# Optimization experiments

Measured on AMD Instinct MI355X. Metric: run time of the kernel, lower is better.

The kernel has to match this reference:

```python
import jax, jax.numpy as jnp
import numpy as np

N = 50000
NEG_SLOPE = 0.2

def _gat_conv(x, src, dst, W, a_src, a_dst, bias, heads, ch):
    # x: [N, F_in]; W: [F_in, heads*ch]; a_src/a_dst: [heads, ch]
    h = (x @ W).reshape(N, heads, ch)                      # [N,H,C]
    e_src = jnp.einsum('nhc,hc->nh', h, a_src)             # [N,H]
    e_dst = jnp.einsum('nhc,hc->nh', h, a_dst)             # [N,H]
    e = jax.nn.leaky_relu(e_src[src] + e_dst[dst], NEG_SLOPE)  # [E,H]
    # segment softmax over destination nodes (self-loops guarantee nonempty segments)
    m = jax.ops.segment_max(e, dst, num_segments=N)        # [N,H]
    p = jnp.exp(e - m[dst])                                # [E,H]
    s = jax.ops.segment_sum(p, dst, num_segments=N)        # [N,H]
    alpha = p / s[dst]                                     # [E,H]
    out = jax.ops.segment_sum(h[src] * alpha[:, :, None], dst, num_segments=N)  # [N,H,C]
    return out.reshape(N, heads * ch) + bias

def _forward(x, src, dst, W1, att_src1, att_dst1, b1, W2, att_src2, att_dst2, b2):
    z = _gat_conv(x, src, dst, W1, att_src1, att_dst1, b1, heads=8, ch=32)
    z = jax.nn.elu(z)
    z = _gat_conv(z, src, dst, W2, att_src2, att_dst2, b2, heads=1, ch=256)
    z = jax.nn.elu(z)
    return z

def setup_inputs() -> dict:
    key = jax.random.key(0)
    ks = jax.random.split(key, 8)
    E = 800000
    x = jax.random.normal(ks[0], (N, 128), dtype=jnp.float32)
    edge_index = jax.random.randint(ks[1], (2, E), 0, N, dtype=jnp.int64)
    g = lambda k, shape: jax.random.normal(k, shape, dtype=jnp.float32) * (1.0 / np.sqrt(shape[0]))
    return {
        'x': x,
        'edge_index': edge_index,
        'W1': g(ks[2], (128, 256)),
        'att_src1': jax.random.normal(ks[3], (8, 32), dtype=jnp.float32) * 0.1,
        'att_dst1': jax.random.normal(ks[4], (8, 32), dtype=jnp.float32) * 0.1,
        'b1': jnp.zeros((256,), dtype=jnp.float32),
        'W2': g(ks[5], (256, 256)),
        'att_src2': jax.random.normal(ks[6], (1, 256), dtype=jnp.float32) * 0.1,
        'att_dst2': jax.random.normal(ks[7], (1, 256), dtype=jnp.float32) * 0.1,
        'b2': jnp.zeros((256,), dtype=jnp.float32),
    }

def reference(x, edge_index, W1, att_src1, att_dst1, b1, W2, att_src2, att_dst2, b2):
    # PyG GATConv default add_self_loops=True: append self-loop edges
    loops = jnp.arange(N, dtype=edge_index.dtype)
    src = jnp.concatenate([edge_index[0], loops])
    dst = jnp.concatenate([edge_index[1], loops])
    return _forward(x, src, dst, W1, att_src1, att_dst1, b1, W2, att_src2, att_dst2, b2)
```

## Files before the change

### kernel.cpp

```cpp
#include <hip/hip_runtime.h>
#include <math.h>

#define N_NODES 50000
#define N_EDGES 800000
#define ET (N_EDGES + N_NODES)
#define D 256
#define NEG_SLOPE 0.2f
#define CAP 56
#define EB ((ET + 255) / 256)
#define XCONV_B ((N_NODES * 128 / 4 + 255) / 256)
#define GEMM_BY ((N_NODES + 127) / 128)

typedef __attribute__((ext_vector_type(8))) _Float16 half8;
typedef __attribute__((ext_vector_type(8))) unsigned short ushort8;
typedef __attribute__((ext_vector_type(4))) unsigned short us4;
typedef __attribute__((ext_vector_type(4))) float f32x4;

__device__ inline unsigned short f2h(float f) {
    union { _Float16 h; unsigned short u; } v; v.h = (_Float16)f; return v.u;
}
__device__ inline float h2f(unsigned short u) {
    union { unsigned short u; _Float16 h; } v; v.u = u; return (float)v.h;
}

__device__ inline int edge_src(const int* eidx, int is32, int e) {
    if (e >= N_EDGES) return e - N_EDGES;
    return is32 ? eidx[e] : eidx[2 * e];
}
__device__ inline int edge_dst(const int* eidx, int is32, int e) {
    if (e >= N_EDGES) return e - N_EDGES;
    return is32 ? eidx[N_EDGES + e] : eidx[2 * (N_EDGES + e)];
}

__global__ __launch_bounds__(256) void init_all(const int* __restrict__ eidx,
                                                int* __restrict__ flag,
                                                int* __restrict__ cnt) {
    int b = blockIdx.x, t = threadIdx.x;
    if (b == 0) {
        __shared__ int any32;
        if (t == 0) any32 = 0;
        __syncthreads();
        int found = 0;
        #pragma unroll
        for (int k = 0; k < 4; ++k) {
            int i = t * 4 + k;
            if (eidx[2 * i + 1] != 0) found = 1;
        }
        if (found) atomicOr(&any32, 1);
        __syncthreads();
        if (t == 0) *flag = any32;
    } else {
        int base = (b - 1) * 1024 + t * 4;
        #pragma unroll
        for (int k = 0; k < 4; ++k) {
            int i = base + k;
            if (i < N_NODES) cnt[i] = 0;
        }
    }
}

__global__ __launch_bounds__(256) void scatter_prep(const int* __restrict__ eidx,
                                                    const int* __restrict__ flag,
                                                    int* __restrict__ cnt,
                                                    int* __restrict__ psrcs,
                                                    const float* __restrict__ W1,
                                                    const float* __restrict__ W2,
                                                    const float* __restrict__ as2,
                                                    const float* __restrict__ ad2,
                                                    const float* __restrict__ x,
                                                    unsigned short* __restrict__ W1t,
                                                    unsigned short* __restrict__ W2t,
                                                    float* __restrict__ was2,
                                                    float* __restrict__ wad2,
                                                    unsigned short* __restrict__ xb) {
    int b = blockIdx.x, t = threadIdx.x;
    if (b < EB) {
        int e = b * 256 + t;
        if (e < ET) {
            int is32 = *flag;
            int src = edge_src(eidx, is32, e);
            int dst = edge_dst(eidx, is32, e);
            int slot = atomicAdd(&cnt[dst], 1);
            psrcs[dst * CAP + slot] = src;
        }
        return;
    }
    b -= EB;
    if (b < 128) {
        W1t[(size_t)t * 128 + b] = f2h(W1[(size_t)b * D + t]);
    } else if (b < 384) {
        int k = b - 128;
        W2t[(size_t)t * D + k] = f2h(W2[(size_t)k * D + t]);
    } else if (b == 384) {
        float s = 0.f, d = 0.f;
        for (int j = 0; j < D; ++j) {
            float w = W2[(size_t)t * D + j];
            s += w * as2[j]; d += w * ad2[j];
        }
        was2[t] = s; wad2[t] = d;
    } else {
        int i = (b - 385) * 256 + t;
        if (i < N_NODES * 128 / 4) {
            float4 v = *(const float4*)&x[(size_t)i * 4];
            us4 o; o.x = f2h(v.x); o.y = f2h(v.y); o.z = f2h(v.z); o.w = f2h(v.w);
            *(us4*)&xb[(size_t)i * 4] = o;
        }
    }
}

template <bool EPI, bool SCORES>
__device__ void gemm_body(int bx, int by,
                          const unsigned short* __restrict__ A,
                          const unsigned short* __restrict__ Bt,
                          void* __restrict__ Cout,
                          const float* __restrict__ bias,
                          const float* __restrict__ a_src,
                          const float* __restrict__ a_dst,
                          float* __restrict__ es,
                          float* __restrict__ ed,
                          int M, int K) {
    __shared__ __align__(16) unsigned short As[128][40];
    __shared__ __align__(16) unsigned short Bs[128][40];
    int t = threadIdx.x, lane = t & 63, wid = t >> 6;
    int wm = wid >> 1, wn = wid & 1;
    int row0 = by * 128, col0 = bx * 128;
    int c15 = lane & 15;
    f32x4 acc[4][4] = {};
    int ar = t >> 1, ap = t & 1;
    for (int k0 = 0; k0 < K; k0 += 32) {
        ushort8 a0 = {0,0,0,0,0,0,0,0}, a1 = {0,0,0,0,0,0,0,0};
        if (row0 + ar < M) {
            const ushort8* p = (const ushort8*)&A[(size_t)(row0 + ar) * K + k0 + ap * 16];
            a0 = p[0]; a1 = p[1];
        }
        *(ushort8*)&As[ar][ap * 16]     = a0;
        *(ushort8*)&As[ar][ap * 16 + 8] = a1;
        const ushort8* q = (const ushort8*)&Bt[(size_t)(col0 + ar) * K + k0 + ap * 16];
        *(ushort8*)&Bs[ar][ap * 16]     = q[0];
        *(ushort8*)&Bs[ar][ap * 16 + 8] = q[1];
        __syncthreads();
        half8 af[4], bg[4];
        #pragma unroll
        for (int mi = 0; mi < 4; ++mi)
            af[mi] = *(const half8*)&As[wm * 64 + mi * 16 + c15][(lane >> 4) * 8];
        #pragma unroll
        for (int ni = 0; ni < 4; ++ni)
            bg[ni] = *(const half8*)&Bs[wn * 64 + ni * 16 + c15][(lane >> 4) * 8];
        #pragma unroll
        for (int mi = 0; mi < 4; ++mi)
            #pragma unroll
            for (int ni = 0; ni < 4; ++ni)
                acc[mi][ni] = __builtin_amdgcn_mfma_f32_16x16x32_f16(af[mi], bg[ni], acc[mi][ni], 0, 0, 0);
        __syncthreads();
    }
    float bcol[4];
    if (EPI) {
        #pragma unroll
        for (int ni = 0; ni < 4; ++ni) bcol[ni] = bias[col0 + wn * 64 + ni * 16 + c15];
    }
    #pragma unroll
    for (int mi = 0; mi < 4; ++mi) {
        int rowb = row0 + wm * 64 + mi * 16 + ((lane >> 4) << 2);
        #pragma unroll
        for (int ni = 0; ni < 4; ++ni) {
            int col = col0 + wn * 64 + ni * 16 + c15;
            #pragma unroll
            for (int r = 0; r < 4; ++r) {
                if (rowb + r >= M) continue;
                if (EPI) {
                    float v = acc[mi][ni][r] + bcol[ni];
                    v = v > 0.f ? v : __expf(v) - 1.f;
                    ((float*)Cout)[(size_t)(rowb + r) * D + col] = v;
                } else {
                    ((unsigned short*)Cout)[(size_t)(rowb + r) * D + col] = f2h(acc[mi][ni][r]);
                }
            }
        }
    }
    if (SCORES) {
        float as_[4], ad_[4];
        #pragma unroll
        for (int ni = 0; ni < 4; ++ni) {
            as_[ni] = a_src[col0 + wn * 64 + ni * 16 + c15];
            ad_[ni] = a_dst[col0 + wn * 64 + ni * 16 + c15];
        }
        int hb0 = bx * 4 + wn * 2;
        #pragma unroll
        for (int mi = 0; mi < 4; ++mi) {
            int rowb = row0 + wm * 64 + mi * 16 + ((lane >> 4) << 2);
            #pragma unroll
            for (int r = 0; r < 4; ++r) {
                float p0 = acc[mi][0][r] * as_[0] + acc[mi][1][r] * as_[1];
                float p1 = acc[mi][2][r] * as_[2] + acc[mi][3][r] * as_[3];
                float q0 = acc[mi][0][r] * ad_[0] + acc[mi][1][r] * ad_[1];
                float q1 = acc[mi][2][r] * ad_[2] + acc[mi][3][r] * ad_[3];
                #pragma unroll
                for (int msk = 1; msk < 16; msk <<= 1) {
                    p0 += __shfl_xor(p0, msk, 64);
                    p1 += __shfl_xor(p1, msk, 64);
                    q0 += __shfl_xor(q0, msk, 64);
                    q1 += __shfl_xor(q1, msk, 64);
                }
                if (c15 == 0 && rowb + r < M) {
                    es[(size_t)(rowb + r) * 8 + hb0]     = p0;
                    es[(size_t)(rowb + r) * 8 + hb0 + 1] = p1;
                    ed[(size_t)(rowb + r) * 8 + hb0]     = q0;
                    ed[(size_t)(rowb + r) * 8 + hb0 + 1] = q1;
                }
            }
        }
    }
}

__global__ __launch_bounds__(256) void gemm1_scores(const unsigned short* __restrict__ xb,
                                                    const unsigned short* __restrict__ W1t,
                                                    unsigned short* __restrict__ hb,
                                                    const float* __restrict__ a_src,
                                                    const float* __restrict__ a_dst,
                                                    float* __restrict__ es,
                                                    float* __restrict__ ed) {
    gemm_body<false, true>(blockIdx.x % 2, blockIdx.x / 2, xb, W1t, hb, nullptr,
                           a_src, a_dst, es, ed, N_NODES, 128);
}

__global__ __launch_bounds__(256) void gemm2_epi(const unsigned short* __restrict__ A,
                                                 const unsigned short* __restrict__ Bt,
                                                 float* __restrict__ Cout,
                                                 const float* __restrict__ bias) {
    gemm_body<true, false>(blockIdx.x % 2, blockIdx.x / 2, A, Bt, Cout, bias,
                           nullptr, nullptr, nullptr, nullptr, N_NODES, 256);
}

__global__ __launch_bounds__(256) void softmax_alpha8(const float* __restrict__ es,
                                                      const float* __restrict__ ed,
                                                      const int* __restrict__ cnt,
                                                      const int* __restrict__ psrcs,
                                                      unsigned short* __restrict__ alpha16) {
    int n = blockIdx.x * 4 + (threadIdx.x >> 6);
    if (n >= N_NODES) return;
    int lane = threadIdx.x & 63;
    int begin = n * CAP, end = begin + cnt[n];
    int j  = lane >> 3;
    int hd = lane & 7;
    float edn = ed[(size_t)n * 8 + hd];
    float m = -1e30f, s = 0.f;
    for (int i = begin + j; i < end; i += 8) {
        float e = es[(size_t)psrcs[i] * 8 + hd] + edn;
        e = e > 0.f ? e : NEG_SLOPE * e;
        float nm = fmaxf(m, e);
        s = s * __expf(m - nm) + __expf(e - nm);
        m = nm;
    }
    #pragma unroll
    for (int mask = 8; mask < 64; mask <<= 1) {
        float om = __shfl_xor(m, mask, 64);
        float os = __shfl_xor(s, mask, 64);
        float nm = fmaxf(m, om);
        s = s * __expf(m - nm) + os * __expf(om - nm);
        m = nm;
    }
    float inv_s = 1.f / s;
    for (int i = begin + j; i < end; i += 8) {
        float e = es[(size_t)psrcs[i] * 8 + hd] + edn;
        e = e > 0.f ? e : NEG_SLOPE * e;
        alpha16[(size_t)i * 8 + hd] = f2h(__expf(e - m) * inv_s);
    }
}

__global__ __launch_bounds__(256) void gather1(const unsigned short* __restrict__ h,
                                               const unsigned short* __restrict__ alpha16,
                                               const int* __restrict__ cnt,
                                               const int* __restrict__ psrcs,
                                               const float* __restrict__ bias,
                                               unsigned short* __restrict__ outh,
                                               const float* __restrict__ was2,
                                               const float* __restrict__ wad2,
                                               float* __restrict__ es2,
                                               float* __restrict__ ed2) {
    int n = blockIdx.x * 4 + (threadIdx.x >> 6);
    if (n >= N_NODES) return;
    int lane = threadIdx.x & 63;
    int begin = n * CAP, end = begin + cnt[n];
    int hsel = lane >> 3;
    float ax = 0.f, ay = 0.f, az = 0.f, aw = 0.f;
    int i = begin;
    for (; i + 7 < end; i += 8) {
        int ss[8]; float w[8]; us4 v[8];
        #pragma unroll
        for (int u = 0; u < 8; ++u) ss[u] = psrcs[i + u];
        #pragma unroll
        for (int u = 0; u < 8; ++u) w[u] = h2f(alpha16[(size_t)(i + u) * 8 + hsel]);
        #pragma unroll
        for (int u = 0; u < 8; ++u) v[u] = *(const us4*)&h[(size_t)ss[u] * D + lane * 4];
        #pragma unroll
        for (int u = 0; u < 8; ++u) {
            ax += h2f(v[u].x) * w[u];
            ay += h2f(v[u].y) * w[u];
            az += h2f(v[u].z) * w[u];
            aw += h2f(v[u].w) * w[u];
        }
    }
    for (; i < end; ++i) {
        int s0 = psrcs[i];
        float w0 = h2f(alpha16[(size_t)i * 8 + hsel]);
        us4 v0 = *(const us4*)&h[(size_t)s0 * D + lane * 4];
        ax += h2f(v0.x) * w0; ay += h2f(v0.y) * w0; az += h2f(v0.z) * w0; aw += h2f(v0.w) * w0;
    }
    float4 b = *(const float4*)&bias[lane * 4];
    float r0 = ax + b.x, r1 = ay + b.y, r2 = az + b.z, r3 = aw + b.w;
    r0 = r0 > 0.f ? r0 : __expf(r0) - 1.f;
    r1 = r1 > 0.f ? r1 : __expf(r1) - 1.f;
    r2 = r2 > 0.f ? r2 : __expf(r2) - 1.f;
    r3 = r3 > 0.f ? r3 : __expf(r3) - 1.f;
    us4 o; o.x = f2h(r0); o.y = f2h(r1); o.z = f2h(r2); o.w = f2h(r3);
    *(us4*)&outh[(size_t)n * D + lane * 4] = o;
    float4 wsv = *(const float4*)&was2[lane * 4];
    float4 wdv = *(const float4*)&wad2[lane * 4];
    float ps = r0 * wsv.x + r1 * wsv.y + r2 * wsv.z + r3 * wsv.w;
    float pd = r0 * wdv.x + r1 * wdv.y + r2 * wdv.z + r3 * wdv.w;
    #pragma unroll
    for (int mask = 1; mask < 64; mask <<= 1) {
        ps += __shfl_xor(ps, mask, 64);
        pd += __shfl_xor(pd, mask, 64);
    }
    if (lane == 0) { es2[n] = ps; ed2[n] = pd; }
}

__global__ __launch_bounds__(256) void gather2_fused(const unsigned short* __restrict__ h,
                                                     const float* __restrict__ es,
                                                     const float* __restrict__ ed,
                                                     const int* __restrict__ cnt,
                                                     const int* __restrict__ psrcs,
                                                     unsigned short* __restrict__ outh) {
    int n = blockIdx.x * 4 + (threadIdx.x >> 6);
    if (n >= N_NODES) return;
    int lane = threadIdx.x & 63;
    int begin = n * CAP;
    int cn = cnt[n];
    float edn = ed[n];
    bool act = lane < cn;
    int sl = act ? psrcs[begin + lane] : 0;
    float el = es[sl] + edn;
    el = el > 0.f ? el : NEG_SLOPE * el;
    float m = act ? el : -1e30f;
    #pragma unroll
    for (int mask = 1; mask < 64; mask <<= 1) m = fmaxf(m, __shfl_xor(m, mask, 64));
    float p = act ? __expf(el - m) : 0.f;
    float ssum = p;
    #pragma unroll
    for (int mask = 1; mask < 64; mask <<= 1) ssum += __shfl_xor(ssum, mask, 64);
    float wl = p / ssum;
    float ax = 0.f, ay = 0.f, az = 0.f, aw = 0.f;
    int j = 0;
    for (; j + 3 < cn; j += 4) {
        int s0 = __shfl(sl, j, 64),     s1 = __shfl(sl, j + 1, 64);
        int s2 = __shfl(sl, j + 2, 64), s3 = __shfl(sl, j + 3, 64);
        float w0 = __shfl(wl, j, 64),     w1 = __shfl(wl, j + 1, 64);
        float w2 = __shfl(wl, j + 2, 64), w3 = __shfl(wl, j + 3, 64);
        us4 v0 = *(const us4*)&h[(size_t)s0 * D + lane * 4];
        us4 v1 = *(const us4*)&h[(size_t)s1 * D + lane * 4];
        us4 v2 = *(const us4*)&h[(size_t)s2 * D + lane * 4];
        us4 v3 = *(const us4*)&h[(size_t)s3 * D + lane * 4];
        ax += h2f(v0.x) * w0 + h2f(v1.x) * w1 + h2f(v2.x) * w2 + h2f(v3.x) * w3;
        ay += h2f(v0.y) * w0 + h2f(v1.y) * w1 + h2f(v2.y) * w2 + h2f(v3.y) * w3;
        az += h2f(v0.z) * w0 + h2f(v1.z) * w1 + h2f(v2.z) * w2 + h2f(v3.z) * w3;
        aw += h2f(v0.w) * w0 + h2f(v1.w) * w1 + h2f(v2.w) * w2 + h2f(v3.w) * w3;
    }
    for (; j < cn; ++j) {
        int s0 = __shfl(sl, j, 64);
        float w0 = __shfl(wl, j, 64);
        us4 v0 = *(const us4*)&h[(size_t)s0 * D + lane * 4];
        ax += h2f(v0.x) * w0; ay += h2f(v0.y) * w0; az += h2f(v0.z) * w0; aw += h2f(v0.w) * w0;
    }
    us4 o; o.x = f2h(ax); o.y = f2h(ay); o.z = f2h(az); o.w = f2h(aw);
    *(us4*)&outh[(size_t)n * D + lane * 4] = o;
}

extern "C" void kernel_launch(void* const* d_in, const int* in_sizes, int n_in,
                              void* d_out, int out_size, void* d_ws, size_t ws_size,
                              hipStream_t stream) {
    const float* x        = (const float*)d_in[0];
    const int*   eidx     = (const int*)d_in[1];
    const float* W1       = (const float*)d_in[2];
    const float* att_src1 = (const float*)d_in[3];
    const float* att_dst1 = (const float*)d_in[4];
    const float* b1       = (const float*)d_in[5];
    const float* W2       = (const float*)d_in[6];
    const float* att_src2 = (const float*)d_in[7];
    const float* att_dst2 = (const float*)d_in[8];
    const float* b2       = (const float*)d_in[9];
    float* out = (float*)d_out;

    char* ws = (char*)d_ws;
    size_t o = 0;
    auto take = [&](size_t bytes) { char* p = ws + o; o = (o + bytes + 255) & ~(size_t)255; return p; };
    unsigned short* hb    = (unsigned short*)take((size_t)N_NODES * D * 2);
    unsigned short* zb    = (unsigned short*)take((size_t)N_NODES * D * 2);
    unsigned short* xb    = (unsigned short*)take((size_t)N_NODES * 128 * 2);
    unsigned short* W1t   = (unsigned short*)take((size_t)D * 128 * 2);
    unsigned short* W2t   = (unsigned short*)take((size_t)D * D * 2);
    unsigned short* alpha16 = (unsigned short*)take((size_t)N_NODES * CAP * 8 * 2);
    float* es1  = (float*)take((size_t)N_NODES * 8 * 4);
    float* ed1  = (float*)take((size_t)N_NODES * 8 * 4);
    float* es2  = (float*)take((size_t)N_NODES * 4);
    float* ed2  = (float*)take((size_t)N_NODES * 4);
    float* was2 = (float*)take(D * 4);
    float* wad2 = (float*)take(D * 4);
    int*   psrcs= (int*)take((size_t)N_NODES * CAP * 4);
    int*   cnt  = (int*)take((size_t)N_NODES * 4);
    int*   flag = (int*)take(256);

    const int NBLK = (N_NODES + 3) / 4;
    const int NB_INIT = (N_NODES + 1023) / 1024;

    init_all<<<1 + NB_INIT, 256, 0, stream>>>(eidx, flag, cnt);
    scatter_prep<<<EB + 385 + XCONV_B, 256, 0, stream>>>(eidx, flag, cnt, psrcs,
                                                         W1, W2, att_src2, att_dst2, x,
                                                         W1t, W2t, was2, wad2, xb);
    gemm1_scores<<<2 * GEMM_BY, 256, 0, stream>>>(xb, W1t, hb, att_src1, att_dst1, es1, ed1);
    softmax_alpha8<<<NBLK, 256, 0, stream>>>(es1, ed1, cnt, psrcs, alpha16);
    gather1<<<NBLK, 256, 0, stream>>>(hb, alpha16, cnt, psrcs, b1, zb, was2, wad2, es2, ed2);
    gather2_fused<<<NBLK, 256, 0, stream>>>(zb, es2, ed2, cnt, psrcs, hb);
    gemm2_epi<<<2 * GEMM_BY, 256, 0, stream>>>(hb, W2t, out, b2);
}
```

Baseline: 275.5 us.

## Fuse edge scatter into layer-1 GEMM kernel to overlap atomics with MFMA

Moves the edge bucketing (atomic count and source scatter) out of the prep kernel and into the layer-1 GEMM kernel. Each GEMM block also handles a contiguous chunk of edges, with odd and even blocks ordering the two phases differently so memory-bound atomic work overlaps compute-bound matrix work. This removes one dependency boundary and lets the atomics hide behind GEMM, at the cost of longer-running, heavier blocks and per-thread strided loops over edges.

```diff
diff --git a/kernel.cpp b/kernel.cpp
--- a/kernel.cpp
+++ b/kernel.cpp
@@ -7,9 +7,10 @@
 #define D 256
 #define NEG_SLOPE 0.2f
 #define CAP 56
-#define EB ((ET + 255) / 256)
 #define XCONV_B ((N_NODES * 128 / 4 + 255) / 256)
 #define GEMM_BY ((N_NODES + 127) / 128)
+#define NSG (2 * GEMM_BY)
+#define EPB ((ET + NSG - 1) / NSG)
 
 typedef __attribute__((ext_vector_type(8))) _Float16 half8;
 typedef __attribute__((ext_vector_type(8))) unsigned short ushort8;
@@ -59,33 +60,17 @@
     }
 }
 
-__global__ __launch_bounds__(256) void scatter_prep(const int* __restrict__ eidx,
-                                                    const int* __restrict__ flag,
-                                                    int* __restrict__ cnt,
-                                                    int* __restrict__ psrcs,
-                                                    const float* __restrict__ W1,
-                                                    const float* __restrict__ W2,
-                                                    const float* __restrict__ as2,
-                                                    const float* __restrict__ ad2,
-                                                    const float* __restrict__ x,
-                                                    unsigned short* __restrict__ W1t,
-                                                    unsigned short* __restrict__ W2t,
-                                                    float* __restrict__ was2,
-                                                    float* __restrict__ wad2,
-                                                    unsigned short* __restrict__ xb) {
+__global__ __launch_bounds__(256) void prep_all(const float* __restrict__ W1,
+                                                const float* __restrict__ W2,
+                                                const float* __restrict__ as2,
+                                                const float* __restrict__ ad2,
+                                                const float* __restrict__ x,
+                                                unsigned short* __restrict__ W1t,
+                                                unsigned short* __restrict__ W2t,
+                                                float* __restrict__ was2,
+                                                float* __restrict__ wad2,
+                                                unsigned short* __restrict__ xb) {
     int b = blockIdx.x, t = threadIdx.x;
-    if (b < EB) {
-        int e = b * 256 + t;
-        if (e < ET) {
-            int is32 = *flag;
-            int src = edge_src(eidx, is32, e);
-            int dst = edge_dst(eidx, is32, e);
-            int slot = atomicAdd(&cnt[dst], 1);
-            psrcs[dst * CAP + slot] = src;
-        }
-        return;
-    }
-    b -= EB;
     if (b < 128) {
         W1t[(size_t)t * 128 + b] = f2h(W1[(size_t)b * D + t]);
     } else if (b < 384) {
@@ -105,6 +90,17 @@
             us4 o; o.x = f2h(v.x); o.y = f2h(v.y); o.z = f2h(v.z); o.w = f2h(v.w);
             *(us4*)&xb[(size_t)i * 4] = o;
         }
+    }
+}
+
+__device__ inline void scatter_chunk(int b, const int* __restrict__ eidx, int is32,
+                                     int* __restrict__ cnt, int* __restrict__ psrcs) {
+    int end = (b + 1) * EPB; if (end > ET) end = ET;
+    for (int e = b * EPB + threadIdx.x; e < end; e += 256) {
+        int src = edge_src(eidx, is32, e);
+        int dst = edge_dst(eidx, is32, e);
+        int slot = atomicAdd(&cnt[dst], 1);
+        psrcs[dst * CAP + slot] = src;
     }
 }
 
@@ -212,15 +208,27 @@
     }
 }
 
-__global__ __launch_bounds__(256) void gemm1_scores(const unsigned short* __restrict__ xb,
-                                                    const unsigned short* __restrict__ W1t,
-                                                    unsigned short* __restrict__ hb,
-                                                    const float* __restrict__ a_src,
-                                                    const float* __restrict__ a_dst,
-                                                    float* __restrict__ es,
-                                                    float* __restrict__ ed) {
-    gemm_body<false, true>(blockIdx.x % 2, blockIdx.x / 2, xb, W1t, hb, nullptr,
-                           a_src, a_dst, es, ed, N_NODES, 128);
+__global__ __launch_bounds__(256) void scatter_gemm1(const int* __restrict__ eidx,
+                                                     const int* __restrict__ flag,
+                                                     int* __restrict__ cnt,
+                                                     int* __restrict__ psrcs,
+                                                     const unsigned short* __restrict__ xb,
+                                                     const unsigned short* __restrict__ W1t,
+                                                     unsigned short* __restrict__ hb,
+                                                     const float* __restrict__ a_src,
+                                                     const float* __restrict__ a_dst,
+                                                     float* __restrict__ es,
+                                                     float* __restrict__ ed) {
+    int b = blockIdx.x;
+    int is32 = *flag;
+    int bx = b & 1, by = b >> 1;
+    if (b & 1) {
+        gemm_body<false, true>(bx, by, xb, W1t, hb, nullptr, a_src, a_dst, es, ed, N_NODES, 128);
+        scatter_chunk(b, eidx, is32, cnt, psrcs);
+    } else {
+        scatter_chunk(b, eidx, is32, cnt, psrcs);
+        gemm_body<false, true>(bx, by, xb, W1t, hb, nullptr, a_src, a_dst, es, ed, N_NODES, 128);
+    }
 }
 
 __global__ __launch_bounds__(256) void gemm2_epi(const unsigned short* __restrict__ A,
@@ -414,10 +422,10 @@
     const int NB_INIT = (N_NODES + 1023) / 1024;
 
     init_all<<<1 + NB_INIT, 256, 0, stream>>>(eidx, flag, cnt);
-    scatter_prep<<<EB + 385 + XCONV_B, 256, 0, stream>>>(eidx, flag, cnt, psrcs,
-                                                         W1, W2, att_src2, att_dst2, x,
-                                                         W1t, W2t, was2, wad2, xb);
-    gemm1_scores<<<2 * GEMM_BY, 256, 0, stream>>>(xb, W1t, hb, att_src1, att_dst1, es1, ed1);
+    prep_all<<<385 + XCONV_B, 256, 0, stream>>>(W1, W2, att_src2, att_dst2, x,
+                                                W1t, W2t, was2, wad2, xb);
+    scatter_gemm1<<<NSG, 256, 0, stream>>>(eidx, flag, cnt, psrcs,
+                                           xb, W1t, hb, att_src1, att_dst1, es1, ed1);
     softmax_alpha8<<<NBLK, 256, 0, stream>>>(es1, ed1, cnt, psrcs, alpha16);
     gather1<<<NBLK, 256, 0, stream>>>(hb, alpha16, cnt, psrcs, b1, zb, was2, wad2, es2, ed2);
     gather2_fused<<<NBLK, 256, 0, stream>>>(zb, es2, ed2, cnt, psrcs, hb);
```

New measurement: 264.6 us. 1.04x faster.

## Slice edge scatter by destination range per XCD and store sources as 16-bit

Applied to the files above, without the earlier changes.

The edge bucketing scatter moves into its own kernel. Each block takes one chunk of edges and keeps only the destinations in one of 8 node slices, chosen by blockIdx & 7, so atomics and writes for a slice likely stay within one XCD's L2. Source indices in the bucket array shrink from int32 to uint16, which halves that array's footprint for the softmax and gather kernels that read it. In exchange each edge is read eight times, there is one more launch, and the code relies on N_NODES fitting in 16 bits; a slot < CAP guard is also added.

```diff
diff --git a/kernel.cpp b/kernel.cpp
--- a/kernel.cpp
+++ b/kernel.cpp
@@ -7,9 +7,11 @@
 #define D 256
 #define NEG_SLOPE 0.2f
 #define CAP 56
-#define EB ((ET + 255) / 256)
 #define XCONV_B ((N_NODES * 128 / 4 + 255) / 256)
 #define GEMM_BY ((N_NODES + 127) / 128)
+#define NCHUNK 256
+#define CE ((ET + NCHUNK - 1) / NCHUNK)
+#define SLICE ((N_NODES + 7) / 8)
 
 typedef __attribute__((ext_vector_type(8))) _Float16 half8;
 typedef __attribute__((ext_vector_type(8))) unsigned short ushort8;
@@ -59,33 +61,17 @@
     }
 }
 
-__global__ __launch_bounds__(256) void scatter_prep(const int* __restrict__ eidx,
-                                                    const int* __restrict__ flag,
-                                                    int* __restrict__ cnt,
-                                                    int* __restrict__ psrcs,
-                                                    const float* __restrict__ W1,
-                                                    const float* __restrict__ W2,
-                                                    const float* __restrict__ as2,
-                                                    const float* __restrict__ ad2,
-                                                    const float* __restrict__ x,
-                                                    unsigned short* __restrict__ W1t,
-                                                    unsigned short* __restrict__ W2t,
-                                                    float* __restrict__ was2,
-                                                    float* __restrict__ wad2,
-                                                    unsigned short* __restrict__ xb) {
+__global__ __launch_bounds__(256) void prep_all(const float* __restrict__ W1,
+                                                const float* __restrict__ W2,
+                                                const float* __restrict__ as2,
+                                                const float* __restrict__ ad2,
+                                                const float* __restrict__ x,
+                                                unsigned short* __restrict__ W1t,
+                                                unsigned short* __restrict__ W2t,
+                                                float* __restrict__ was2,
+                                                float* __restrict__ wad2,
+                                                unsigned short* __restrict__ xb) {
     int b = blockIdx.x, t = threadIdx.x;
-    if (b < EB) {
-        int e = b * 256 + t;
-        if (e < ET) {
-            int is32 = *flag;
-            int src = edge_src(eidx, is32, e);
-            int dst = edge_dst(eidx, is32, e);
-            int slot = atomicAdd(&cnt[dst], 1);
-            psrcs[dst * CAP + slot] = src;
-        }
-        return;
-    }
-    b -= EB;
     if (b < 128) {
         W1t[(size_t)t * 128 + b] = f2h(W1[(size_t)b * D + t]);
     } else if (b < 384) {
@@ -104,6 +90,25 @@
             float4 v = *(const float4*)&x[(size_t)i * 4];
             us4 o; o.x = f2h(v.x); o.y = f2h(v.y); o.z = f2h(v.z); o.w = f2h(v.w);
             *(us4*)&xb[(size_t)i * 4] = o;
+        }
+    }
+}
+
+__global__ __launch_bounds__(256) void scatter_sliced(const int* __restrict__ eidx,
+                                                      const int* __restrict__ flag,
+                                                      int* __restrict__ cnt,
+                                                      unsigned short* __restrict__ psrcs) {
+    int b = blockIdx.x;
+    int s = b & 7, c = b >> 3;
+    int is32 = *flag;
+    int lo = s * SLICE, hi = lo + SLICE; if (hi > N_NODES) hi = N_NODES;
+    int e1 = (c + 1) * CE; if (e1 > ET) e1 = ET;
+    for (int e = c * CE + threadIdx.x; e < e1; e += 256) {
+        int dst = edge_dst(eidx, is32, e);
+        if (dst >= lo && dst < hi) {
+            int src = edge_src(eidx, is32, e);
+            int slot = atomicAdd(&cnt[dst], 1);
+            if (slot < CAP) psrcs[dst * CAP + slot] = (unsigned short)src;
         }
     }
 }
@@ -234,7 +239,7 @@
 __global__ __launch_bounds__(256) void softmax_alpha8(const float* __restrict__ es,
                                                       const float* __restrict__ ed,
                                                       const int* __restrict__ cnt,
-                                                      const int* __restrict__ psrcs,
+                                                      const unsigned short* __restrict__ psrcs,
                                                       unsigned short* __restrict__ alpha16) {
     int n = blockIdx.x * 4 + (threadIdx.x >> 6);
     if (n >= N_NODES) return;
@@ -270,7 +275,7 @@
 __global__ __launch_bounds__(256) void gather1(const unsigned short* __restrict__ h,
                                                const unsigned short* __restrict__ alpha16,
                                                const int* __restrict__ cnt,
-                                               const int* __restrict__ psrcs,
+                                               const unsigned short* __restrict__ psrcs,
                                                const float* __restrict__ bias,
                                                unsigned short* __restrict__ outh,
                                                const float* __restrict__ was2,
@@ -330,7 +335,7 @@
                                                      const float* __restrict__ es,
                                                      const float* __restrict__ ed,
                                                      const int* __restrict__ cnt,
-                                                     const int* __restrict__ psrcs,
+                                                     const unsigned short* __restrict__ psrcs,
                                                      unsigned short* __restrict__ outh) {
     int n = blockIdx.x * 4 + (threadIdx.x >> 6);
     if (n >= N_NODES) return;
@@ -339,7 +344,7 @@
     int cn = cnt[n];
     float edn = ed[n];
     bool act = lane < cn;
-    int sl = act ? psrcs[begin + lane] : 0;
+    int sl = act ? (int)psrcs[begin + lane] : 0;
     float el = es[sl] + edn;
     el = el > 0.f ? el : NEG_SLOPE * el;
     float m = act ? el : -1e30f;
@@ -406,7 +411,7 @@
     float* ed2  = (float*)take((size_t)N_NODES * 4);
     float* was2 = (float*)take(D * 4);
     float* wad2 = (float*)take(D * 4);
-    int*   psrcs= (int*)take((size_t)N_NODES * CAP * 4);
+    unsigned short* psrcs = (unsigned short*)take((size_t)N_NODES * CAP * 2);
     int*   cnt  = (int*)take((size_t)N_NODES * 4);
     int*   flag = (int*)take(256);
 
@@ -414,9 +419,9 @@
     const int NB_INIT = (N_NODES + 1023) / 1024;
 
     init_all<<<1 + NB_INIT, 256, 0, stream>>>(eidx, flag, cnt);
-    scatter_prep<<<EB + 385 + XCONV_B, 256, 0, stream>>>(eidx, flag, cnt, psrcs,
-                                                         W1, W2, att_src2, att_dst2, x,
-                                                         W1t, W2t, was2, wad2, xb);
+    prep_all<<<385 + XCONV_B, 256, 0, stream>>>(W1, W2, att_src2, att_dst2, x,
+                                                W1t, W2t, was2, wad2, xb);
+    scatter_sliced<<<8 * NCHUNK, 256, 0, stream>>>(eidx, flag, cnt, psrcs);
     gemm1_scores<<<2 * GEMM_BY, 256, 0, stream>>>(xb, W1t, hb, att_src1, att_dst1, es1, ed1);
     softmax_alpha8<<<NBLK, 256, 0, stream>>>(es1, ed1, cnt, psrcs, alpha16);
     gather1<<<NBLK, 256, 0, stream>>>(hb, alpha16, cnt, psrcs, b1, zb, was2, wad2, es2, ed2);
```

After: 263.6 us. 4.3% less time.
